# Optimization experiments

Measured on AMD Instinct MI355X. Metric: run time of the kernel, lower is better.

Reference implementation:

```python
import jax, jax.numpy as jnp
import numpy as np

B, T, C, H = 4, 2048, 1024, 8
D = C // H


def _rope_tables(t, d, base=10000.0):
    inv = 1.0 / (base ** (jnp.arange(0, d, 2, dtype=jnp.float32) / d))
    freqs = jnp.outer(jnp.arange(t, dtype=jnp.float32), inv)  # (T, D/2)
    cos = jnp.concatenate([jnp.cos(freqs)] * 2, axis=-1)  # (T, D)
    sin = jnp.concatenate([jnp.sin(freqs)] * 2, axis=-1)
    return cos, sin


def _apply_rope(x, cos, sin):
    # x: (B,H,T,D); rotate-half RoPE
    d2 = x.shape[-1] // 2
    x1, x2 = x[..., :d2], x[..., d2:]
    rot = jnp.concatenate([-x2, x1], axis=-1)
    return x * cos + rot * sin


def setup_inputs() -> dict:
    key = jax.random.key(0)
    ks = jax.random.split(key, 8)
    x = jax.random.normal(ks[0], (B, T, C), jnp.float32)
    w = lambda k: jax.random.normal(k, (C, C), jnp.float32) * 0.02
    # trigram directions: 8 sign patterns in {-1,+1}^3, L2-normalized (as in get_trigrams + F.normalize)
    signs = np.array([[(1 if (i >> b) & 1 else -1) for b in range(3)] for i in range(8)], np.float32)
    head_dirs = jnp.asarray(signs / np.sqrt(3.0))
    return {
        'x': x,
        'Wq': w(ks[1]), 'Wk': w(ks[2]), 'Wv': w(ks[3]), 'Wo': w(ks[4]),
        'ln_g': jnp.ones((C,), jnp.float32), 'ln_b': jnp.zeros((C,), jnp.float32),
        'head_scales': jax.random.normal(ks[5], (H,), jnp.float32) * 0.1,
        'head_dirs': head_dirs,
    }


def reference(x, Wq, Wk, Wv, Wo, ln_g, ln_b, head_scales, head_dirs):
    b, t, c = x.shape
    h = head_dirs.shape[0]
    d = c // h
    scale = 1.0 / jnp.sqrt(jnp.asarray(d, x.dtype))
    # pre-LN
    mu = jnp.mean(x, axis=-1, keepdims=True)
    var = jnp.mean((x - mu) ** 2, axis=-1, keepdims=True)
    xn = (x - mu) * jax.lax.rsqrt(var + 1e-5) * ln_g + ln_b
    q = (xn @ Wq.T).reshape(b, t, h, d).transpose(0, 2, 1, 3)  # (B,H,T,D)
    k = (xn @ Wk.T).reshape(b, t, h, d).transpose(0, 2, 1, 3)
    v = (xn @ Wv.T).reshape(b, t, h, d).transpose(0, 2, 1, 3)
    cos, sin = _rope_tables(t, d)
    q = _apply_rope(q, cos, sin)
    k = _apply_rope(k, cos, sin)
    causal = jnp.tril(jnp.ones((t, t), bool))
    # standard causal SDPA
    scores = jnp.einsum('bhqd,bhkd->bhqk', q, k) * scale
    scores = jnp.where(causal, scores, -jnp.inf)
    attn = jax.nn.softmax(scores, axis=-1)
    out = jnp.einsum('bhqk,bhkd->bhqd', attn, v)
    # trigram geometric bias attention (rank-1 logits from first 3 dims)
    qp = jnp.einsum('bhtd,hd->bht', q[..., :3], head_dirs)
    kp = jnp.einsum('bhtd,hd->bht', k[..., :3], head_dirs)
    geo = qp[..., :, None] * kp[..., None, :]  # (B,H,T,T)
    geo = jnp.where(causal, geo, -jnp.inf)
    geo_attn = jax.nn.softmax(geo, axis=-1)
    geo_out = jnp.einsum('bhqk,bhkd->bhqd', geo_attn, v)
    out = out + head_scales[None, :, None, None] * jax.lax.stop_gradient(geo_out - out)
    out = out.transpose(0, 2, 1, 3).reshape(b, t, c) @ Wo.T
    return x + out
```

## Files before the change

kernel.cpp:

```cpp
#include <hip/hip_runtime.h>
#include <hip/hip_bf16.h>
#include <stdint.h>

#define BB 4
#define TT 2048
#define CC 1024
#define HH 8
#define DD 128

typedef unsigned short u16;
typedef unsigned int u32;
typedef unsigned long long u64;
typedef __attribute__((ext_vector_type(4))) float f32x4;
typedef __attribute__((ext_vector_type(16))) float f32x16;
typedef __attribute__((ext_vector_type(8))) __bf16 bf16x8;

__device__ __forceinline__ float bf2f(u16 u){ u32 x=((u32)u)<<16; float f; __builtin_memcpy(&f,&x,4); return f; }
__device__ __forceinline__ u16 f2bf(float f){ u32 x; __builtin_memcpy(&x,&f,4); x += 0x7fffu + ((x>>16)&1u); return (u16)(x>>16); }

__device__ __forceinline__ void gload16(const void* g, void* l){
  __builtin_amdgcn_global_load_lds((const __attribute__((address_space(1))) u32*)g,
                                   (__attribute__((address_space(3))) u32*)l, 16, 0, 0);
}
__device__ __forceinline__ f32x4 mfma16(bf16x8 a, bf16x8 b, f32x4 c){
  return __builtin_amdgcn_mfma_f32_16x16x32_bf16(a,b,c,0,0,0);
}
__device__ __forceinline__ f32x16 mfma32(bf16x8 a, bf16x8 b, f32x16 c){
  return __builtin_amdgcn_mfma_f32_32x32x16_bf16(a,b,c,0,0,0);
}
__device__ __forceinline__ u32 cvtpk(float lo, float hi){
  u32 r; asm("v_cvt_pk_bf16_f32 %0, %1, %2" : "=v"(r) : "v"(lo), "v"(hi)); return r;
}
__device__ __forceinline__ void pl32swap(u32& d, u32& s){
  asm volatile("v_permlane32_swap_b32 %0, %1" : "+v"(d), "+v"(s));
}
union FRAG { u32 u[4]; bf16x8 v; };

__global__ void ln_k(const float* __restrict__ x, const float* __restrict__ g,
                     const float* __restrict__ bta, u16* __restrict__ xn){
  int row = blockIdx.x, tid = threadIdx.x;
  const float4 v = ((const float4*)(x + (size_t)row*CC))[tid];
  float s = v.x+v.y+v.z+v.w;
  float ss = v.x*v.x+v.y*v.y+v.z*v.z+v.w*v.w;
  #pragma unroll
  for(int m=1;m<64;m<<=1){ s += __shfl_xor(s,m); ss += __shfl_xor(ss,m); }
  __shared__ float red[8];
  if((tid&63)==0){ red[tid>>6]=s; red[4+(tid>>6)]=ss; }
  __syncthreads();
  float ts = red[0]+red[1]+red[2]+red[3];
  float tss = red[4]+red[5]+red[6]+red[7];
  float mu = ts*(1.0f/CC);
  float rs = rsqrtf(tss*(1.0f/CC) - mu*mu + 1e-5f);
  int c0 = tid*4;
  ushort4 o;
  o.x = f2bf((v.x-mu)*rs*g[c0+0]+bta[c0+0]);
  o.y = f2bf((v.y-mu)*rs*g[c0+1]+bta[c0+1]);
  o.z = f2bf((v.z-mu)*rs*g[c0+2]+bta[c0+2]);
  o.w = f2bf((v.w-mu)*rs*g[c0+3]+bta[c0+3]);
  ((ushort4*)(xn + (size_t)row*CC))[tid] = o;
}

__global__ void wconv_k(const float* __restrict__ wq, const float* __restrict__ wk,
                        const float* __restrict__ wv, const float* __restrict__ wo,
                        u16* __restrict__ out){
  int i = blockIdx.x*256 + threadIdx.x;
  int sel = i>>18;
  const float* src = sel==0?wq: sel==1?wk: sel==2?wv:wo;
  float4 v = ((const float4*)src)[i & 262143];
  ushort4 o; o.x=f2bf(v.x); o.y=f2bf(v.y); o.z=f2bf(v.z); o.w=f2bf(v.w);
  ((ushort4*)out)[i] = o;
}

__global__ void rope_tab_k(float* __restrict__ cosT, float* __restrict__ sinT){
  int i = blockIdx.x*256 + threadIdx.x;
  int t = i>>6, j = i&63;
  float inv = powf(10000.0f, -(float)(2*j)*(1.0f/128.0f));
  float a = (float)t * inv;
  cosT[i] = cosf(a);
  sinT[i] = sinf(a);
}

__global__ void qpkp_k(const u16* __restrict__ Qb, const u16* __restrict__ Kb,
                       const float* __restrict__ dirs, const float* __restrict__ cosT,
                       const float* __restrict__ sinT, float* __restrict__ qp, float* __restrict__ kp){
  int idx = blockIdx.x*256 + threadIdx.x;
  int b = idx>>14, rem = idx & 16383;
  int h = rem>>11, t = rem & 2047;
  size_t base = ((size_t)(b*TT + t))*CC + h*DD;
  float qv = 0.f, kv = 0.f;
  #pragma unroll
  for(int d=0; d<3; d++){
    float c = cosT[t*64+d], s = sinT[t*64+d];
    float dr = dirs[h*3+d];
    qv += (bf2f(Qb[base+d])*c - bf2f(Qb[base+d+64])*s) * dr;
    kv += (bf2f(Kb[base+d])*c - bf2f(Kb[base+d+64])*s) * dr;
  }
  qp[idx] = qv; kp[idx] = kv;
}

__global__ void ropepack_k(u16* __restrict__ Qb, const u16* __restrict__ Kb,
                           u16* __restrict__ KF,
                           const float* __restrict__ cosT, const float* __restrict__ sinT){
  int bt = blockIdx.x, tid = threadIdx.x;
  int b = bt>>11, t = bt & (TT-1);
  int ks = t>>5, k31 = t&31;
  #pragma unroll
  for(int pp=0; pp<4; pp++){
    int p = tid*4+pp;
    int h = p>>6, d = p&63;
    size_t i1 = (size_t)bt*CC + h*DD + d;
    float c = cosT[t*64+d], s = sinT[t*64+d];
    float q1 = bf2f(Qb[i1]), q2 = bf2f(Qb[i1+64]);
    Qb[i1]    = f2bf(q1*c - q2*s);
    Qb[i1+64] = f2bf(q2*c + q1*s);
    float k1 = bf2f(Kb[i1]), k2 = bf2f(Kb[i1+64]);
    u16 kr1 = f2bf(k1*c - k2*s);
    u16 kr2 = f2bf(k2*c + k1*s);
    int bh = b*HH + h;
    int d2 = d + 64;
    size_t o1 = (((size_t)(bh*64 + ks)*8) + (d >>4))*512 + (((d >>3)&1)*32 + k31)*8 + (d &7);
    size_t o2 = (((size_t)(bh*64 + ks)*8) + (d2>>4))*512 + (((d2>>3)&1)*32 + k31)*8 + (d2&7);
    KF[o1] = kr1;
    KF[o2] = kr2;
  }
}

template<int MODE>
__global__ __launch_bounds__(256) void gemm_k(const u16* __restrict__ A, const u16* __restrict__ W,
                                              u16* __restrict__ outb, float* __restrict__ outf,
                                              const float* __restrict__ resid){
  __shared__ __align__(16) u16 As[128*64];
  __shared__ __align__(16) u16 Bs[128*64];
  const int K = CC;
  int m0 = blockIdx.x*128, n0 = blockIdx.y*128;
  int tid = threadIdx.x, w = tid>>6, l = tid&63;
  int li = l&15, lg = l>>4;
  int wm = w>>1, wn = w&1;
  f32x4 acc[4][4] = {};
  for(int k0=0; k0<K; k0+=64){
    #pragma unroll
    for(int i=0;i<4;i++){
      int L = (w*4+i)*1024 + l*16;
      int row = L>>7;
      int colb = (L&127) ^ ((row&7)<<4);
      gload16(A + ((size_t)(m0+row)*K + k0 + (colb>>1)), (char*)As + (w*4+i)*1024);
      gload16(W + ((size_t)(n0+row)*K + k0 + (colb>>1)), (char*)Bs + (w*4+i)*1024);
    }
    __syncthreads();
    #pragma unroll
    for(int kc=0;kc<2;kc++){
      bf16x8 af[4], bfr[4];
      #pragma unroll
      for(int mi=0;mi<4;mi++){
        int row = wm*64 + mi*16 + li;
        int colb = (kc*64 + lg*16) ^ ((row&7)<<4);
        af[mi] = *(const bf16x8*)((const char*)As + row*128 + colb);
      }
      #pragma unroll
      for(int ni=0;ni<4;ni++){
        int row = wn*64 + ni*16 + li;
        int colb = (kc*64 + lg*16) ^ ((row&7)<<4);
        bfr[ni] = *(const bf16x8*)((const char*)Bs + row*128 + colb);
      }
      #pragma unroll
      for(int mi=0;mi<4;mi++){
        #pragma unroll
        for(int ni=0;ni<4;ni++)
          acc[mi][ni] = mfma16(af[mi], bfr[ni], acc[mi][ni]);
      }
    }
    __syncthreads();
  }
  #pragma unroll
  for(int mi=0;mi<4;mi++){
    #pragma unroll
    for(int ni=0;ni<4;ni++){
      #pragma unroll
      for(int r=0;r<4;r++){
        int row = m0 + wm*64 + mi*16 + lg*4 + r;
        int col = n0 + wn*64 + ni*16 + li;
        float v = acc[mi][ni][r];
        if(MODE==0){
          outb[(size_t)row*CC + col] = f2bf(v);
        } else if(MODE==4){
          int t = row & 2047, b = row>>11;
          int h = col>>7, d = col&127;
          int bh = b*HH + h;
          size_t o = (((size_t)(bh*64 + (t>>5))*8) + (d>>5)*2 + ((t>>4)&1))*512
                     + (((t>>3)&1)*32 + (d&31))*8 + (t&7);
          outb[o] = f2bf(v);
        } else {
          size_t o = (size_t)row*CC + col;
          outf[o] = v + resid[o];
        }
      }
    }
  }
}

struct SegState { float m1, l1, m2, l2; f32x16 a1[4]; f32x16 a2[4]; };

__device__ __forceinline__ void run_seg(int t, int klo, int khi, int bh, int b, int h,
                                        int l5, int q31,
                                        const u16* __restrict__ Q, const u16* __restrict__ KF,
                                        const u16* __restrict__ VF, const float* __restrict__ qp,
                                        const float* __restrict__ kp, SegState& S){
  const f32x16 zf = {};
  S.m1 = -__builtin_inff(); S.l1 = 0.f; S.m2 = -__builtin_inff(); S.l2 = 0.f;
  #pragma unroll
  for(int dt=0;dt<4;dt++){ S.a1[dt] = zf; S.a2[dt] = zf; }
  if(khi <= klo) return;

  int q0 = t*32, q = q0 + q31;
  bf16x8 qf[8];
  {
    const u16* qbase = Q + ((size_t)(b*TT + q)*CC + h*DD);
    #pragma unroll
    for(int db=0;db<8;db++) qf[db] = *(const bf16x8*)(qbase + db*16 + l5*8);
  }
  const float L2E = 1.442695040888963f;
  const float sl2 = 0.08838834764831845f * L2E;
  bf16x8 qpf;
  {
    float qs = qp[(size_t)bh*TT + q] * L2E;
    u16 qh = f2bf(qs); float qhf = bf2f(qh);
    u16 ql = f2bf(qs - qhf);
    FRAG fq; fq.u[0] = l5? 0u : ((u32)qh | ((u32)qh<<16));
    fq.u[1] = l5? 0u : (u32)ql; fq.u[2]=0; fq.u[3]=0;
    qpf = fq.v;
  }
  const u16* kfp = KF + (size_t)bh*64*4096 + (size_t)klo*4096 + (size_t)(q31 + 32*l5)*8;
  const u16* vfp = VF + (size_t)bh*64*4096 + (size_t)klo*4096 + (size_t)(q31 + 32*l5)*8;
  const float* kpp = kp + (size_t)bh*TT + q31;

  for(int is=klo; is<khi; ++is){
    int ksub = is*32;

    bf16x8 kf0 = *(const bf16x8*)(kfp + 0*512);
    bf16x8 kf1 = *(const bf16x8*)(kfp + 1*512);
    bf16x8 kf2 = *(const bf16x8*)(kfp + 2*512);
    bf16x8 kf3 = *(const bf16x8*)(kfp + 3*512);
    bf16x8 kf4 = *(const bf16x8*)(kfp + 4*512);
    bf16x8 kf5 = *(const bf16x8*)(kfp + 5*512);
    bf16x8 kf6 = *(const bf16x8*)(kfp + 6*512);
    bf16x8 kf7 = *(const bf16x8*)(kfp + 7*512);

    f32x16 s0 = zf, s1a = zf;
    __builtin_amdgcn_s_setprio(1);
    s0  = mfma32(kf0, qf[0], s0);  s1a = mfma32(kf1, qf[1], s1a);
    s0  = mfma32(kf2, qf[2], s0);  s1a = mfma32(kf3, qf[3], s1a);
    s0  = mfma32(kf4, qf[4], s0);  s1a = mfma32(kf5, qf[5], s1a);
    s0  = mfma32(kf6, qf[6], s0);  s1a = mfma32(kf7, qf[7], s1a);
    __builtin_amdgcn_s_setprio(0);

    f32x16 gg;
    {
      float kpv = kpp[ksub];
      u16 kh = f2bf(kpv); float khf = bf2f(kh);
      u16 kl = f2bf(kpv - khf);
      FRAG fk; fk.u[0] = l5? 0u : ((u32)kh | ((u32)kl<<16));
      fk.u[1] = l5? 0u : (u32)kh; fk.u[2]=0; fk.u[3]=0;
      gg = mfma32(fk.v, qpf, zf);
    }

    float sv[16], gv[16];
    #pragma unroll
    for(int rr=0;rr<16;rr++){ sv[rr] = (s0[rr]+s1a[rr])*sl2; gv[rr] = gg[rr]; }
    if(ksub + 31 > q0){
      #pragma unroll
      for(int rr=0;rr<16;rr++){
        int kg = ksub + (rr&3) + 8*(rr>>2) + 4*l5;
        if(kg > q){ sv[rr] = -__builtin_inff(); gv[rr] = -__builtin_inff(); }
      }
    }

    float mx=-__builtin_inff(), gx=-__builtin_inff();
    #pragma unroll
    for(int rr=0;rr<16;rr++){ mx = fmaxf(mx, sv[rr]); gx = fmaxf(gx, gv[rr]); }
    mx = fmaxf(mx, __shfl_xor(mx,32));
    gx = fmaxf(gx, __shfl_xor(gx,32));
    if(__ballot((mx > S.m1+8.f) | (gx > S.m2+8.f))){
      float mn1 = fmaxf(S.m1,mx), mn2 = fmaxf(S.m2,gx);
      float c1 = exp2f(S.m1-mn1), c2 = exp2f(S.m2-mn2);
      S.l1 *= c1; S.l2 *= c2; S.m1 = mn1; S.m2 = mn2;
      #pragma unroll
      for(int dt=0;dt<4;dt++){ S.a1[dt] *= c1; S.a2[dt] *= c2; }
    }
    float rs1=0.f, rs2=0.f;
    float e1[16], e2[16];
    #pragma unroll
    for(int rr=0;rr<16;rr++){
      e1[rr] = exp2f(sv[rr] - S.m1); rs1 += e1[rr];
      e2[rr] = exp2f(gv[rr] - S.m2); rs2 += e2[rr];
    }
    rs1 += __shfl_xor(rs1,32); rs2 += __shfl_xor(rs2,32);
    S.l1 += rs1; S.l2 += rs2;

    u32 P1[8], P2[8];
    #pragma unroll
    for(int m=0;m<8;m++){ P1[m] = cvtpk(e1[2*m], e1[2*m+1]); P2[m] = cvtpk(e2[2*m], e2[2*m+1]); }
    pl32swap(P1[0],P1[2]); pl32swap(P1[1],P1[3]); pl32swap(P1[4],P1[6]); pl32swap(P1[5],P1[7]);
    pl32swap(P2[0],P2[2]); pl32swap(P2[1],P2[3]); pl32swap(P2[4],P2[6]); pl32swap(P2[5],P2[7]);

    #pragma unroll
    for(int kb2=0;kb2<2;kb2++){
      FRAG f1, f2;
      #pragma unroll
      for(int j2=0;j2<4;j2++){ f1.u[j2] = P1[kb2*4+j2]; f2.u[j2] = P2[kb2*4+j2]; }
      bf16x8 pb1 = f1.v, pb2 = f2.v;
      bf16x8 vf0 = *(const bf16x8*)(vfp + (0+kb2)*512);
      bf16x8 vf1 = *(const bf16x8*)(vfp + (2+kb2)*512);
      bf16x8 vf2 = *(const bf16x8*)(vfp + (4+kb2)*512);
      bf16x8 vf3 = *(const bf16x8*)(vfp + (6+kb2)*512);
      __builtin_amdgcn_s_setprio(1);
      S.a1[0] = mfma32(vf0, pb1, S.a1[0]);  S.a2[0] = mfma32(vf0, pb2, S.a2[0]);
      S.a1[1] = mfma32(vf1, pb1, S.a1[1]);  S.a2[1] = mfma32(vf1, pb2, S.a2[1]);
      S.a1[2] = mfma32(vf2, pb1, S.a1[2]);  S.a2[2] = mfma32(vf2, pb2, S.a2[2]);
      S.a1[3] = mfma32(vf3, pb1, S.a1[3]);  S.a2[3] = mfma32(vf3, pb2, S.a2[3]);
      __builtin_amdgcn_s_setprio(0);
    }
    kfp += 4096; vfp += 4096;
  }
}

__global__ __launch_bounds__(128,2) void attn_k(const u16* __restrict__ Q, const u16* __restrict__ KF,
                                                const u16* __restrict__ VF, const float* __restrict__ qp,
                                                const float* __restrict__ kp, const float* __restrict__ hs,
                                                u16* __restrict__ outp){
  __shared__ __align__(16) float lp1[4*64*16];
  __shared__ __align__(16) float lp2[4*64*16];
  __shared__ float lml[32*4];
  int bid = blockIdx.x;
  int xcd = bid&7, r = bid>>3;
  int bh = xcd*4 + (r&3);
  int p = r>>2;
  int b = bh>>3, h = bh&7;
  int tid = threadIdx.x, w = tid>>6, l = tid&63;
  int l5 = l>>5, q31 = l&31;
  float sh = hs[h];

  SegState S;
  if(w==0){
    run_seg(p, 0, p+1, bh, b, h, l5, q31, Q, KF, VF, qp, kp, S);
    {
      float rl1 = 1.0f/S.l1, rl2 = 1.0f/S.l2;
      int q = p*32 + q31;
      u16* obase = outp + (size_t)(b*TT + q)*CC + h*DD;
      #pragma unroll
      for(int dt=0;dt<4;dt++){
        #pragma unroll
        for(int m=0;m<8;m++){
          float oa1 = S.a1[dt][2*m]*rl1,   oa2 = S.a2[dt][2*m]*rl2;
          float ob1 = S.a1[dt][2*m+1]*rl1, ob2 = S.a2[dt][2*m+1]*rl2;
          float oa = oa1 + sh*(oa2-oa1);
          float ob = ob1 + sh*(ob2-ob1);
          int d = dt*32 + (2*m&3) + 8*(m>>1) + 4*l5;
          *(u32*)(obase + d) = cvtpk(oa, ob);
        }
      }
    }
    run_seg(63-p, 0, 31-p, bh, b, h, l5, q31, Q, KF, VF, qp, kp, S);
    #pragma unroll
    for(int dt=0;dt<4;dt++){
      *(f32x16*)&lp1[(dt*64 + l)*16] = S.a1[dt];
      *(f32x16*)&lp2[(dt*64 + l)*16] = S.a2[dt];
    }
    if(l5==0){
      lml[q31*4+0] = S.m1; lml[q31*4+1] = S.l1;
      lml[q31*4+2] = S.m2; lml[q31*4+3] = S.l2;
    }
    __syncthreads();
  } else {
    run_seg(63-p, 31-p, 64-p, bh, b, h, l5, q31, Q, KF, VF, qp, kp, S);
    __syncthreads();
    float mA1 = lml[q31*4+0], lA1 = lml[q31*4+1];
    float mA2 = lml[q31*4+2], lA2 = lml[q31*4+3];
    float M1 = fmaxf(mA1, S.m1), M2 = fmaxf(mA2, S.m2);
    float wA1 = exp2f(mA1-M1), wB1 = exp2f(S.m1-M1);
    float wA2 = exp2f(mA2-M2), wB2 = exp2f(S.m2-M2);
    float r1 = 1.0f/(wA1*lA1 + wB1*S.l1);
    float r2 = 1.0f/(wA2*lA2 + wB2*S.l2);
    int q = (63-p)*32 + q31;
    u16* obase = outp + (size_t)(b*TT + q)*CC + h*DD;
    #pragma unroll
    for(int dt=0;dt<4;dt++){
      f32x16 pa1 = *(const f32x16*)&lp1[(dt*64 + l)*16];
      f32x16 pa2 = *(const f32x16*)&lp2[(dt*64 + l)*16];
      #pragma unroll
      for(int m=0;m<8;m++){
        float oa1 = (wA1*pa1[2*m]   + wB1*S.a1[dt][2*m])*r1;
        float ob1 = (wA1*pa1[2*m+1] + wB1*S.a1[dt][2*m+1])*r1;
        float oa2 = (wA2*pa2[2*m]   + wB2*S.a2[dt][2*m])*r2;
        float ob2 = (wA2*pa2[2*m+1] + wB2*S.a2[dt][2*m+1])*r2;
        float oa = oa1 + sh*(oa2-oa1);
        float ob = ob1 + sh*(ob2-ob1);
        int d = dt*32 + (2*m&3) + 8*(m>>1) + 4*l5;
        *(u32*)(obase + d) = cvtpk(oa, ob);
      }
    }
  }
}

extern "C" void kernel_launch(void* const* d_in, const int* in_sizes, int n_in,
                              void* d_out, int out_size, void* d_ws, size_t ws_size,
                              hipStream_t stream){
  (void)in_sizes; (void)n_in; (void)out_size; (void)ws_size;
  const float* x   = (const float*)d_in[0];
  const float* Wq  = (const float*)d_in[1];
  const float* Wk  = (const float*)d_in[2];
  const float* Wv  = (const float*)d_in[3];
  const float* Wo  = (const float*)d_in[4];
  const float* lng = (const float*)d_in[5];
  const float* lnb = (const float*)d_in[6];
  const float* hsc = (const float*)d_in[7];
  const float* hdr = (const float*)d_in[8];

  char* ws = (char*)d_ws;
  const size_t MB = 1048576;
  u16* xn   = (u16*)ws;
  u16* wbf  = (u16*)(ws + 16*MB);
  u16* Qb   = (u16*)(ws + 24*MB);
  u16* Kb   = (u16*)(ws + 40*MB);
  u16* VF   = (u16*)(ws + 56*MB);
  u16* KF   = (u16*)(ws + 72*MB);
  float* cosT = (float*)(ws + 88*MB);
  float* sinT = cosT + 131072;
  float* qp   = sinT + 131072;
  float* kp   = qp + 65536;

  ln_k<<<8192,256,0,stream>>>(x, lng, lnb, xn);
  wconv_k<<<4096,256,0,stream>>>(Wq,Wk,Wv,Wo,wbf);
  rope_tab_k<<<512,256,0,stream>>>(cosT,sinT);
  gemm_k<0><<<dim3(64,8),256,0,stream>>>(xn, wbf,          Qb, nullptr, nullptr);
  gemm_k<0><<<dim3(64,8),256,0,stream>>>(xn, wbf+1048576,  Kb, nullptr, nullptr);
  gemm_k<4><<<dim3(64,8),256,0,stream>>>(xn, wbf+2097152,  VF, nullptr, nullptr);
  qpkp_k<<<256,256,0,stream>>>(Qb,Kb,hdr,cosT,sinT,qp,kp);
  ropepack_k<<<8192,128,0,stream>>>(Qb,Kb,KF,cosT,sinT);
  attn_k<<<1024,128,0,stream>>>(Qb,KF,VF,qp,kp,hsc,xn);
  gemm_k<2><<<dim3(64,8),256,0,stream>>>(xn, wbf+3145728, nullptr, (float*)d_out, x);
}
```

Measured before the change: 231.6 us.

## Split each query tile's KV range across two waves and halve merge LDS

The attention kernel now launches one block per 32-row query tile, ordered heaviest first, instead of pairing tile p with tile 63-p. The two waves split that tile's key range in half and merge through a single LDS buffer in two passes, which halves shared memory. The softmax scale is folded into Q during RoPE packing, which removes a multiply per score in the inner loop. Small tiles now leave one wave nearly idle and there are more blocks, but lower LDS use may allow higher occupancy.

```diff
diff --git a/kernel.cpp b/kernel.cpp
--- a/kernel.cpp
+++ b/kernel.cpp
@@ -101,6 +101,7 @@
 __global__ void ropepack_k(u16* __restrict__ Qb, const u16* __restrict__ Kb,
                            u16* __restrict__ KF,
                            const float* __restrict__ cosT, const float* __restrict__ sinT){
+  const float SL2 = 0.08838834764831845f * 1.442695040888963f;
   int bt = blockIdx.x, tid = threadIdx.x;
   int b = bt>>11, t = bt & (TT-1);
   int ks = t>>5, k31 = t&31;
@@ -111,8 +112,8 @@
     size_t i1 = (size_t)bt*CC + h*DD + d;
     float c = cosT[t*64+d], s = sinT[t*64+d];
     float q1 = bf2f(Qb[i1]), q2 = bf2f(Qb[i1+64]);
-    Qb[i1]    = f2bf(q1*c - q2*s);
-    Qb[i1+64] = f2bf(q2*c + q1*s);
+    Qb[i1]    = f2bf((q1*c - q2*s)*SL2);
+    Qb[i1+64] = f2bf((q2*c + q1*s)*SL2);
     float k1 = bf2f(Kb[i1]), k2 = bf2f(Kb[i1+64]);
     u16 kr1 = f2bf(k1*c - k2*s);
     u16 kr2 = f2bf(k2*c + k1*s);
@@ -219,7 +220,6 @@
     for(int db=0;db<8;db++) qf[db] = *(const bf16x8*)(qbase + db*16 + l5*8);
   }
   const float L2E = 1.442695040888963f;
-  const float sl2 = 0.08838834764831845f * L2E;
   bf16x8 qpf;
   {
     float qs = qp[(size_t)bh*TT + q] * L2E;
@@ -265,7 +265,7 @@
 
     float sv[16], gv[16];
     #pragma unroll
-    for(int rr=0;rr<16;rr++){ sv[rr] = (s0[rr]+s1a[rr])*sl2; gv[rr] = gg[rr]; }
+    for(int rr=0;rr<16;rr++){ sv[rr] = s0[rr]+s1a[rr]; gv[rr] = gg[rr]; }
     if(ksub + 31 > q0){
       #pragma unroll
       for(int rr=0;rr<16;rr++){
@@ -327,73 +327,63 @@
                                                 const u16* __restrict__ VF, const float* __restrict__ qp,
                                                 const float* __restrict__ kp, const float* __restrict__ hs,
                                                 u16* __restrict__ outp){
-  __shared__ __align__(16) float lp1[4*64*16];
-  __shared__ __align__(16) float lp2[4*64*16];
+  __shared__ __align__(16) float bufA[4*64*16];
   __shared__ float lml[32*4];
   int bid = blockIdx.x;
   int xcd = bid&7, r = bid>>3;
   int bh = xcd*4 + (r&3);
-  int p = r>>2;
+  int j = 63 - (r>>2);
   int b = bh>>3, h = bh&7;
   int tid = threadIdx.x, w = tid>>6, l = tid&63;
   int l5 = l>>5, q31 = l&31;
+  int n = j+1, a = n>>1;
+  int klo = w? a : 0, khi = w? n : a;
   float sh = hs[h];
 
   SegState S;
+  run_seg(j, klo, khi, bh, b, h, l5, q31, Q, KF, VF, qp, kp, S);
+
   if(w==0){
-    run_seg(p, 0, p+1, bh, b, h, l5, q31, Q, KF, VF, qp, kp, S);
-    {
-      float rl1 = 1.0f/S.l1, rl2 = 1.0f/S.l2;
-      int q = p*32 + q31;
-      u16* obase = outp + (size_t)(b*TT + q)*CC + h*DD;
-      #pragma unroll
-      for(int dt=0;dt<4;dt++){
-        #pragma unroll
-        for(int m=0;m<8;m++){
-          float oa1 = S.a1[dt][2*m]*rl1,   oa2 = S.a2[dt][2*m]*rl2;
-          float ob1 = S.a1[dt][2*m+1]*rl1, ob2 = S.a2[dt][2*m+1]*rl2;
-          float oa = oa1 + sh*(oa2-oa1);
-          float ob = ob1 + sh*(ob2-ob1);
-          int d = dt*32 + (2*m&3) + 8*(m>>1) + 4*l5;
-          *(u32*)(obase + d) = cvtpk(oa, ob);
-        }
-      }
-    }
-    run_seg(63-p, 0, 31-p, bh, b, h, l5, q31, Q, KF, VF, qp, kp, S);
-    #pragma unroll
-    for(int dt=0;dt<4;dt++){
-      *(f32x16*)&lp1[(dt*64 + l)*16] = S.a1[dt];
-      *(f32x16*)&lp2[(dt*64 + l)*16] = S.a2[dt];
-    }
+    #pragma unroll
+    for(int dt=0;dt<4;dt++) *(f32x16*)&bufA[(dt*64 + l)*16] = S.a1[dt];
     if(l5==0){
       lml[q31*4+0] = S.m1; lml[q31*4+1] = S.l1;
       lml[q31*4+2] = S.m2; lml[q31*4+3] = S.l2;
     }
-    __syncthreads();
-  } else {
-    run_seg(63-p, 31-p, 64-p, bh, b, h, l5, q31, Q, KF, VF, qp, kp, S);
-    __syncthreads();
+  }
+  __syncthreads();
+  float wA2=0.f, wB2=0.f, r2=0.f;
+  if(w==1){
     float mA1 = lml[q31*4+0], lA1 = lml[q31*4+1];
     float mA2 = lml[q31*4+2], lA2 = lml[q31*4+3];
     float M1 = fmaxf(mA1, S.m1), M2 = fmaxf(mA2, S.m2);
     float wA1 = exp2f(mA1-M1), wB1 = exp2f(S.m1-M1);
-    float wA2 = exp2f(mA2-M2), wB2 = exp2f(S.m2-M2);
+    wA2 = exp2f(mA2-M2); wB2 = exp2f(S.m2-M2);
     float r1 = 1.0f/(wA1*lA1 + wB1*S.l1);
-    float r2 = 1.0f/(wA2*lA2 + wB2*S.l2);
-    int q = (63-p)*32 + q31;
+    r2 = 1.0f/(wA2*lA2 + wB2*S.l2);
+    #pragma unroll
+    for(int dt=0;dt<4;dt++){
+      f32x16 pa = *(const f32x16*)&bufA[(dt*64 + l)*16];
+      S.a1[dt] = (S.a1[dt]*wB1 + pa*wA1)*r1;
+    }
+  }
+  __syncthreads();
+  if(w==0){
+    #pragma unroll
+    for(int dt=0;dt<4;dt++) *(f32x16*)&bufA[(dt*64 + l)*16] = S.a2[dt];
+  }
+  __syncthreads();
+  if(w==1){
+    int q = j*32 + q31;
     u16* obase = outp + (size_t)(b*TT + q)*CC + h*DD;
     #pragma unroll
     for(int dt=0;dt<4;dt++){
-      f32x16 pa1 = *(const f32x16*)&lp1[(dt*64 + l)*16];
-      f32x16 pa2 = *(const f32x16*)&lp2[(dt*64 + l)*16];
+      f32x16 pa = *(const f32x16*)&bufA[(dt*64 + l)*16];
+      f32x16 o2v = (S.a2[dt]*wB2 + pa*wA2)*r2;
       #pragma unroll
       for(int m=0;m<8;m++){
-        float oa1 = (wA1*pa1[2*m]   + wB1*S.a1[dt][2*m])*r1;
-        float ob1 = (wA1*pa1[2*m+1] + wB1*S.a1[dt][2*m+1])*r1;
-        float oa2 = (wA2*pa2[2*m]   + wB2*S.a2[dt][2*m])*r2;
-        float ob2 = (wA2*pa2[2*m+1] + wB2*S.a2[dt][2*m+1])*r2;
-        float oa = oa1 + sh*(oa2-oa1);
-        float ob = ob1 + sh*(ob2-ob1);
+        float oa = S.a1[dt][2*m]   + sh*(o2v[2*m]   - S.a1[dt][2*m]);
+        float ob = S.a1[dt][2*m+1] + sh*(o2v[2*m+1] - S.a1[dt][2*m+1]);
         int d = dt*32 + (2*m&3) + 8*(m>>1) + 4*l5;
         *(u32*)(obase + d) = cvtpk(oa, ob);
       }
@@ -436,6 +426,6 @@
   gemm_k<4><<<dim3(64,8),256,0,stream>>>(xn, wbf+2097152,  VF, nullptr, nullptr);
   qpkp_k<<<256,256,0,stream>>>(Qb,Kb,hdr,cosT,sinT,qp,kp);
   ropepack_k<<<8192,128,0,stream>>>(Qb,Kb,KF,cosT,sinT);
-  attn_k<<<1024,128,0,stream>>>(Qb,KF,VF,qp,kp,hsc,xn);
+  attn_k<<<2048,128,0,stream>>>(Qb,KF,VF,qp,kp,hsc,xn);
   gemm_k<2><<<dim3(64,8),256,0,stream>>>(xn, wbf+3145728, nullptr, (float*)d_out, x);
 }
```

After: 233.5 us. No clear change (+0.8%).

## Double-buffer K/V tiles in LDS via async global loads; fold softmax scale into Q

Applied to the files above, without the earlier changes.

The attention loop now stages each 32-key K and V tile into per-wave LDS double buffers with global_load_lds. The next tile is prefetched while the current one is consumed, with explicit vmcnt waits, instead of issuing direct global fragment loads every iteration. This is meant to hide global memory latency behind the MFMA and softmax work. The scale and log2(e) multiply is moved into the RoPE pack step that writes Q, which removes a per-score multiply but rounds the pre-scaled Q to bf16. Shared memory grows to about 66 KB per block, and the reduction scratch now aliases wave 0's staging buffers, which may limit occupancy.

```diff
diff --git a/kernel.cpp b/kernel.cpp
--- a/kernel.cpp
+++ b/kernel.cpp
@@ -101,6 +101,7 @@
 __global__ void ropepack_k(u16* __restrict__ Qb, const u16* __restrict__ Kb,
                            u16* __restrict__ KF,
                            const float* __restrict__ cosT, const float* __restrict__ sinT){
+  const float SL2 = 0.08838834764831845f * 1.442695040888963f;
   int bt = blockIdx.x, tid = threadIdx.x;
   int b = bt>>11, t = bt & (TT-1);
   int ks = t>>5, k31 = t&31;
@@ -111,8 +112,8 @@
     size_t i1 = (size_t)bt*CC + h*DD + d;
     float c = cosT[t*64+d], s = sinT[t*64+d];
     float q1 = bf2f(Qb[i1]), q2 = bf2f(Qb[i1+64]);
-    Qb[i1]    = f2bf(q1*c - q2*s);
-    Qb[i1+64] = f2bf(q2*c + q1*s);
+    Qb[i1]    = f2bf((q1*c - q2*s)*SL2);
+    Qb[i1+64] = f2bf((q2*c + q1*s)*SL2);
     float k1 = bf2f(Kb[i1]), k2 = bf2f(Kb[i1+64]);
     u16 kr1 = f2bf(k1*c - k2*s);
     u16 kr2 = f2bf(k2*c + k1*s);
@@ -201,7 +202,8 @@
 struct SegState { float m1, l1, m2, l2; f32x16 a1[4]; f32x16 a2[4]; };
 
 __device__ __forceinline__ void run_seg(int t, int klo, int khi, int bh, int b, int h,
-                                        int l5, int q31,
+                                        int l5, int q31, int l,
+                                        char* bufA, char* bufB,
                                         const u16* __restrict__ Q, const u16* __restrict__ KF,
                                         const u16* __restrict__ VF, const float* __restrict__ qp,
                                         const float* __restrict__ kp, SegState& S){
@@ -219,7 +221,6 @@
     for(int db=0;db<8;db++) qf[db] = *(const bf16x8*)(qbase + db*16 + l5*8);
   }
   const float L2E = 1.442695040888963f;
-  const float sl2 = 0.08838834764831845f * L2E;
   bf16x8 qpf;
   {
     float qs = qp[(size_t)bh*TT + q] * L2E;
@@ -229,23 +230,45 @@
     fq.u[1] = l5? 0u : (u32)ql; fq.u[2]=0; fq.u[3]=0;
     qpf = fq.v;
   }
-  const u16* kfp = KF + (size_t)bh*64*4096 + (size_t)klo*4096 + (size_t)(q31 + 32*l5)*8;
-  const u16* vfp = VF + (size_t)bh*64*4096 + (size_t)klo*4096 + (size_t)(q31 + 32*l5)*8;
+  const u16* kfsrc = KF + (size_t)bh*64*4096 + (size_t)klo*4096 + (size_t)l*8;
+  const u16* vfsrc = VF + (size_t)bh*64*4096 + (size_t)klo*4096 + (size_t)l*8;
   const float* kpp = kp + (size_t)bh*TT + q31;
+
+  auto stage = [&](const u16* ks, const u16* vs, char* dst){
+    #pragma unroll
+    for(int c=0;c<8;c++) gload16(ks + c*512, dst + c*1024);
+    #pragma unroll
+    for(int c=0;c<8;c++) gload16(vs + c*512, dst + 8192 + c*1024);
+  };
+
+  stage(kfsrc, vfsrc, bufA);
+  kfsrc += 4096; vfsrc += 4096;
+  char* cur = bufA; char* nxt = bufB;
 
   for(int is=klo; is<khi; ++is){
     int ksub = is*32;
-
-    bf16x8 kf0 = *(const bf16x8*)(kfp + 0*512);
-    bf16x8 kf1 = *(const bf16x8*)(kfp + 1*512);
-    bf16x8 kf2 = *(const bf16x8*)(kfp + 2*512);
-    bf16x8 kf3 = *(const bf16x8*)(kfp + 3*512);
-    bf16x8 kf4 = *(const bf16x8*)(kfp + 4*512);
-    bf16x8 kf5 = *(const bf16x8*)(kfp + 5*512);
-    bf16x8 kf6 = *(const bf16x8*)(kfp + 6*512);
-    bf16x8 kf7 = *(const bf16x8*)(kfp + 7*512);
-
-    f32x16 s0 = zf, s1a = zf;
+    float kpv = kpp[ksub];
+    if(is+1 < khi){
+      stage(kfsrc, vfsrc, nxt);
+      kfsrc += 4096; vfsrc += 4096;
+      asm volatile("s_waitcnt vmcnt(16)" ::: "memory");
+    } else {
+      asm volatile("s_waitcnt vmcnt(0)" ::: "memory");
+    }
+    __builtin_amdgcn_sched_barrier(0);
+
+    const u16* kbuf = (const u16*)cur;
+    const u16* vbuf = (const u16*)(cur + 8192);
+    bf16x8 kf0 = *(const bf16x8*)(kbuf + 0*512 + l*8);
+    bf16x8 kf1 = *(const bf16x8*)(kbuf + 1*512 + l*8);
+    bf16x8 kf2 = *(const bf16x8*)(kbuf + 2*512 + l*8);
+    bf16x8 kf3 = *(const bf16x8*)(kbuf + 3*512 + l*8);
+    bf16x8 kf4 = *(const bf16x8*)(kbuf + 4*512 + l*8);
+    bf16x8 kf5 = *(const bf16x8*)(kbuf + 5*512 + l*8);
+    bf16x8 kf6 = *(const bf16x8*)(kbuf + 6*512 + l*8);
+    bf16x8 kf7 = *(const bf16x8*)(kbuf + 7*512 + l*8);
+
+    f32x16 s0 = {}, s1a = {};
     __builtin_amdgcn_s_setprio(1);
     s0  = mfma32(kf0, qf[0], s0);  s1a = mfma32(kf1, qf[1], s1a);
     s0  = mfma32(kf2, qf[2], s0);  s1a = mfma32(kf3, qf[3], s1a);
@@ -255,17 +278,17 @@
 
     f32x16 gg;
     {
-      float kpv = kpp[ksub];
+      const f32x16 zf2 = {};
       u16 kh = f2bf(kpv); float khf = bf2f(kh);
       u16 kl = f2bf(kpv - khf);
       FRAG fk; fk.u[0] = l5? 0u : ((u32)kh | ((u32)kl<<16));
       fk.u[1] = l5? 0u : (u32)kh; fk.u[2]=0; fk.u[3]=0;
-      gg = mfma32(fk.v, qpf, zf);
+      gg = mfma32(fk.v, qpf, zf2);
     }
 
     float sv[16], gv[16];
     #pragma unroll
-    for(int rr=0;rr<16;rr++){ sv[rr] = (s0[rr]+s1a[rr])*sl2; gv[rr] = gg[rr]; }
+    for(int rr=0;rr<16;rr++){ sv[rr] = s0[rr]+s1a[rr]; gv[rr] = gg[rr]; }
     if(ksub + 31 > q0){
       #pragma unroll
       for(int rr=0;rr<16;rr++){
@@ -308,10 +331,10 @@
       #pragma unroll
       for(int j2=0;j2<4;j2++){ f1.u[j2] = P1[kb2*4+j2]; f2.u[j2] = P2[kb2*4+j2]; }
       bf16x8 pb1 = f1.v, pb2 = f2.v;
-      bf16x8 vf0 = *(const bf16x8*)(vfp + (0+kb2)*512);
-      bf16x8 vf1 = *(const bf16x8*)(vfp + (2+kb2)*512);
-      bf16x8 vf2 = *(const bf16x8*)(vfp + (4+kb2)*512);
-      bf16x8 vf3 = *(const bf16x8*)(vfp + (6+kb2)*512);
+      bf16x8 vf0 = *(const bf16x8*)(vbuf + (0+kb2)*512 + l*8);
+      bf16x8 vf1 = *(const bf16x8*)(vbuf + (2+kb2)*512 + l*8);
+      bf16x8 vf2 = *(const bf16x8*)(vbuf + (4+kb2)*512 + l*8);
+      bf16x8 vf3 = *(const bf16x8*)(vbuf + (6+kb2)*512 + l*8);
       __builtin_amdgcn_s_setprio(1);
       S.a1[0] = mfma32(vf0, pb1, S.a1[0]);  S.a2[0] = mfma32(vf0, pb2, S.a2[0]);
       S.a1[1] = mfma32(vf1, pb1, S.a1[1]);  S.a2[1] = mfma32(vf1, pb2, S.a2[1]);
@@ -319,7 +342,7 @@
       S.a1[3] = mfma32(vf3, pb1, S.a1[3]);  S.a2[3] = mfma32(vf3, pb2, S.a2[3]);
       __builtin_amdgcn_s_setprio(0);
     }
-    kfp += 4096; vfp += 4096;
+    { char* tmp = cur; cur = nxt; nxt = tmp; }
   }
 }
 
@@ -327,9 +350,10 @@
                                                 const u16* __restrict__ VF, const float* __restrict__ qp,
                                                 const float* __restrict__ kp, const float* __restrict__ hs,
                                                 u16* __restrict__ outp){
-  __shared__ __align__(16) float lp1[4*64*16];
-  __shared__ __align__(16) float lp2[4*64*16];
-  __shared__ float lml[32*4];
+  __shared__ __align__(16) char smem[66048];
+  float* lp1 = (float*)smem;
+  float* lp2 = (float*)(smem + 16384);
+  float* lml = (float*)(smem + 65536);
   int bid = blockIdx.x;
   int xcd = bid&7, r = bid>>3;
   int bh = xcd*4 + (r&3);
@@ -337,11 +361,13 @@
   int b = bh>>3, h = bh&7;
   int tid = threadIdx.x, w = tid>>6, l = tid&63;
   int l5 = l>>5, q31 = l&31;
+  char* bufA = smem + w*32768;
+  char* bufB = bufA + 16384;
   float sh = hs[h];
 
   SegState S;
   if(w==0){
-    run_seg(p, 0, p+1, bh, b, h, l5, q31, Q, KF, VF, qp, kp, S);
+    run_seg(p, 0, p+1, bh, b, h, l5, q31, l, bufA, bufB, Q, KF, VF, qp, kp, S);
     {
       float rl1 = 1.0f/S.l1, rl2 = 1.0f/S.l2;
       int q = p*32 + q31;
@@ -359,7 +385,7 @@
         }
       }
     }
-    run_seg(63-p, 0, 31-p, bh, b, h, l5, q31, Q, KF, VF, qp, kp, S);
+    run_seg(63-p, 0, 31-p, bh, b, h, l5, q31, l, bufA, bufB, Q, KF, VF, qp, kp, S);
     #pragma unroll
     for(int dt=0;dt<4;dt++){
       *(f32x16*)&lp1[(dt*64 + l)*16] = S.a1[dt];
@@ -371,7 +397,7 @@
     }
     __syncthreads();
   } else {
-    run_seg(63-p, 31-p, 64-p, bh, b, h, l5, q31, Q, KF, VF, qp, kp, S);
+    run_seg(63-p, 31-p, 64-p, bh, b, h, l5, q31, l, bufA, bufB, Q, KF, VF, qp, kp, S);
     __syncthreads();
     float mA1 = lml[q31*4+0], lA1 = lml[q31*4+1];
     float mA2 = lml[q31*4+2], lA2 = lml[q31*4+3];
```

After: 278.2 us. +20.1%, slower.
